# Kernel optimization log

Measured on AMD Instinct MI355X. Metric: run time of the kernel, lower is better.

The kernel has to match this reference:

```python
import jax, jax.numpy as jnp
import numpy as np

BS, SL, D_IN, D_MODEL, H = 4, 128, 512, 512, 8
DP = D_MODEL // H


def setup_inputs() -> dict:
    key = jax.random.key(0)
    ks = jax.random.split(key, 12)
    s = 0.02
    inp = {
        "q": jax.random.normal(ks[0], (BS, SL, D_IN), jnp.float32),
        "k": jax.random.normal(ks[1], (BS, SL, D_IN), jnp.float32),
        "v": jax.random.normal(ks[2], (BS, SL, D_IN), jnp.float32),
    }
    j = jnp.arange(SL)
    # mask[t, jk] = 1.0 for the zero-padded slots jk > t in the shuffled sequence for step t
    mask2d = (j[None, :] > j[:, None]).astype(jnp.float32)  # (SL, SL)
    inp["mask"] = mask2d[None, :, None, None, :]            # (1, SL, 1, 1, SL)
    for i, n in enumerate(["wq", "wk", "wv", "dense"]):
        din = D_IN if n != "dense" else D_MODEL
        inp[n + "_w"] = jax.random.normal(ks[3 + 2 * i], (din, D_MODEL), jnp.float32) * s
        inp[n + "_b"] = jnp.zeros((D_MODEL,), jnp.float32)
    return inp


def _shuffle_idx(key, sl):
    # Row t of returned idx: random permutation of [0..t-1], then t, then t+1.. (padding slots).
    u = jax.random.uniform(key, (sl, sl))
    j = jnp.arange(sl)
    t = j[:, None]
    sort_keys = jnp.where(j[None, :] < t, u, j[None, :].astype(jnp.float32) + 2.0)
    return jnp.argsort(sort_keys, axis=-1)  # (sl, sl) int32


def _split_heads_shuffled(x, idx, valid):
    # x: (bs, sl, d) -> (bs, sl, H, sl, DP); padding slots (j > t) zeroed like torch plc_holder
    bs, sl, d = x.shape
    xt = x[:, idx, :] * valid[None, :, :, None]  # (bs, sl, sl, d)
    xt = xt.reshape(bs, sl, sl, H, DP)
    return xt.transpose(0, 1, 3, 2, 4)


def reference(q, k, v, mask, wq_w, wq_b, wk_w, wk_b, wv_w, wv_b, dense_w, dense_b):
    bs, sl, _ = q.shape
    j = jnp.arange(sl)
    valid = (j[None, :] <= j[:, None]).astype(q.dtype)  # (sl, sl)
    pkey = jax.random.key(42)
    idx_q = _shuffle_idx(jax.random.fold_in(pkey, 0), sl)
    idx_k = _shuffle_idx(jax.random.fold_in(pkey, 1), sl)
    idx_v = _shuffle_idx(jax.random.fold_in(pkey, 2), sl)

    qp = q @ wq_w + wq_b
    kp = k @ wk_w + wk_b
    vp = v @ wv_w + wv_b

    qh = _split_heads_shuffled(qp, idx_q, valid)  # (bs, sl, H, sl, DP)
    kh = _split_heads_shuffled(kp, idx_k, valid)
    vh = _split_heads_shuffled(vp, idx_v, valid)

    logits = jnp.einsum('bthqd,bthkd->bthqk', qh, kh) / jnp.sqrt(jnp.float32(DP))
    logits = logits + mask * (-1e9)
    attn = jax.nn.softmax(logits, axis=-1)          # (bs, sl, H, sl, sl)
    ctx = jnp.einsum('bthqk,bthkd->bthqd', attn, vh)  # (bs, sl, H, sl, DP)

    ctx = ctx.transpose(0, 1, 3, 2, 4).reshape(bs, sl, sl, H * DP)
    eff = ctx[:, j, j, :]                           # query row t of step t (the token itself)
    out = eff @ dense_w + dense_b                   # (bs, sl, d_model); dropout p=0 -> identity
    return (out, attn)
```

## Files before the change

kernel.cpp:

```cpp
#include <hip/hip_runtime.h>
#include <stdint.h>


#define BSZ 4
#define SLEN 128
#define DMODEL 512
#define NHEAD 8
#define HDIM 64

typedef float f32x4_t __attribute__((ext_vector_type(4)));

__device__ __forceinline__ uint32_t rotl32(uint32_t v, int d) {
  return (v << d) | (v >> (32 - d));
}

__device__ __forceinline__ void tf2x32(uint32_t k0, uint32_t k1, uint32_t x0,
                                       uint32_t x1, uint32_t& y0, uint32_t& y1) {
  uint32_t ks2 = k0 ^ k1 ^ 0x1BD11BDAu;
  x0 += k0; x1 += k1;
#define TF_R(r) { x0 += x1; x1 = rotl32(x1, (r)); x1 ^= x0; }
  TF_R(13) TF_R(15) TF_R(26) TF_R(6)
  x0 += k1;  x1 += ks2 + 1u;
  TF_R(17) TF_R(29) TF_R(16) TF_R(24)
  x0 += ks2; x1 += k0 + 2u;
  TF_R(13) TF_R(15) TF_R(26) TF_R(6)
  x0 += k0;  x1 += k1 + 3u;
  TF_R(17) TF_R(29) TF_R(16) TF_R(24)
  x0 += k1;  x1 += ks2 + 4u;
  TF_R(13) TF_R(15) TF_R(26) TF_R(6)
  x0 += ks2; x1 += k0 + 5u;
#undef TF_R
  y0 = x0; y1 = x1;
}

__device__ __forceinline__ uint16_t f32_to_bf16(float v) {
  uint32_t x = __float_as_uint(v);
  return (uint16_t)((x + 0x7FFFu + ((x >> 16) & 1u)) >> 16);
}
__device__ __forceinline__ float bf16_to_f32(uint16_t b) {
  return __uint_as_float(((uint32_t)b) << 16);
}

__global__ __launch_bounds__(128) void idx_kernel(int* __restrict__ idx) {
  const int m = blockIdx.x;
  const int t = blockIdx.y;
  const int j = threadIdx.x;
  __shared__ float u[SLEN];
  uint32_t fk0, fk1;
  tf2x32(0u, 42u, 0u, (uint32_t)m, fk0, fk1);
  const int flat = t * SLEN + j;
  uint32_t y0, y1;
  tf2x32(fk0, fk1, 0u, (uint32_t)flat, y0, y1);
  uint32_t bits = y0 ^ y1;
  float uu = __uint_as_float((bits >> 9) | 0x3f800000u) - 1.0f;
  u[j] = uu;
  __syncthreads();
  int* row = idx + (m * SLEN + t) * SLEN;
  if (j >= t) {
    row[j] = j;
  } else {
    int rank = 0;
    for (int i = 0; i < t; ++i) {
      float ui = u[i];
      rank += ((ui < uu) || (ui == uu && i < j)) ? 1 : 0;
    }
    row[rank] = j;
  }
}

__device__ __forceinline__ void gemm512_body(const float* __restrict__ A,
                                             const float* __restrict__ W,
                                             const float* __restrict__ bias,
                                             float* __restrict__ C,
                                             float* As , float* Ws ) {
  const int tid = threadIdx.x;
  const int tx = tid & 15;
  const int ty = tid >> 4;
  const int row0 = blockIdx.y * 32, col0 = blockIdx.x * 64;
  const int lr = tid >> 2, lc = (tid & 3) << 2;
  const int wr = tid >> 4, wc = (tid & 15) << 2;
  float acc[2][4] = {};
  float4 av, wv;
  if (tid < 128) av = *(const float4*)(A + (size_t)(row0 + lr) * 512 + lc);
  wv = *(const float4*)(W + (size_t)wr * 512 + col0 + wc);
  for (int k0 = 0; k0 < 512; k0 += 16) {
    if (tid < 128) {
      As[lr * 17 + lc + 0] = av.x; As[lr * 17 + lc + 1] = av.y;
      As[lr * 17 + lc + 2] = av.z; As[lr * 17 + lc + 3] = av.w;
    }
    *(float4*)(Ws + wr * 64 + wc) = wv;
    __syncthreads();
    if (k0 + 16 < 512) {
      if (tid < 128) av = *(const float4*)(A + (size_t)(row0 + lr) * 512 + k0 + 16 + lc);
      wv = *(const float4*)(W + (size_t)(k0 + 16 + wr) * 512 + col0 + wc);
    }
#pragma unroll
    for (int kk = 0; kk < 16; ++kk) {
      float a0 = As[(ty * 2 + 0) * 17 + kk];
      float a1 = As[(ty * 2 + 1) * 17 + kk];
      float bvv[4];
#pragma unroll
      for (int jj = 0; jj < 4; ++jj) bvv[jj] = Ws[kk * 64 + tx * 4 + jj];
#pragma unroll
      for (int jj = 0; jj < 4; ++jj) {
        acc[0][jj] += a0 * bvv[jj];
        acc[1][jj] += a1 * bvv[jj];
      }
    }
    __syncthreads();
  }
#pragma unroll
  for (int i = 0; i < 2; ++i) {
    int r = row0 + ty * 2 + i, c = col0 + tx * 4;
    float4 o;
    o.x = acc[i][0] + bias[c + 0];
    o.y = acc[i][1] + bias[c + 1];
    o.z = acc[i][2] + bias[c + 2];
    o.w = acc[i][3] + bias[c + 3];
    *(float4*)(C + (size_t)r * 512 + c) = o;
  }
}

__global__ __launch_bounds__(256) void proj_kernel(
    const float* __restrict__ q, const float* __restrict__ k, const float* __restrict__ v,
    const float* __restrict__ wq, const float* __restrict__ wk, const float* __restrict__ wv,
    const float* __restrict__ bq, const float* __restrict__ bk, const float* __restrict__ bv,
    float* __restrict__ qp, float* __restrict__ kp, float* __restrict__ vp) {
  __shared__ float As[32 * 17];
  __shared__ float Ws[16 * 64];
  const float* A; const float* W; const float* B; float* C;
  if (blockIdx.z == 0)      { A = q; W = wq; B = bq; C = qp; }
  else if (blockIdx.z == 1) { A = k; W = wk; B = bk; C = kp; }
  else                      { A = v; W = wv; B = bv; C = vp; }
  gemm512_body(A, W, B, C, As, Ws);
}

__global__ __launch_bounds__(256) void dense_kernel(const float* __restrict__ A,
                                                    const float* __restrict__ W,
                                                    const float* __restrict__ B,
                                                    float* __restrict__ C) {
  __shared__ float As[32 * 17];
  __shared__ float Ws[16 * 64];
  gemm512_body(A, W, B, C, As, Ws);
}

__global__ __launch_bounds__(256) void sef_kernel(const float* __restrict__ qp,
                                                  const float* __restrict__ kp,
                                                  uint16_t* __restrict__ E,
                                                  float* __restrict__ Ft) {
  const int h = blockIdx.x, b = blockIdx.y, qc = blockIdx.z;
  const int tid = threadIdx.x;
  __shared__ float qs[32 * 36];
  __shared__ float ks[32 * 132];
  __shared__ float redm[32 * 16];
  __shared__ float csum[32 * 16];
  __shared__ float m32s[32];
  const float* qbase = qp + ((size_t)(b * SLEN + qc * 32)) * DMODEL + h * HDIM;
  const float* kbase = kp + ((size_t)b * SLEN) * DMODEL + h * HDIM;
  const int i0 = (tid >> 4) * 2, jg = tid & 15, j0 = jg * 8;
  float acc[2][8] = {};
  for (int d0 = 0; d0 < HDIM; d0 += 32) {
    __syncthreads();
    {
      int row = tid >> 3, c4 = (tid & 7) << 2;
      float4 a = *(const float4*)(qbase + (size_t)row * DMODEL + d0 + c4);
      qs[(c4 + 0) * 36 + row] = a.x; qs[(c4 + 1) * 36 + row] = a.y;
      qs[(c4 + 2) * 36 + row] = a.z; qs[(c4 + 3) * 36 + row] = a.w;
    }
    for (int it = 0; it < 4; ++it) {
      int flat = it * 256 + tid;
      int row = flat >> 3, c4 = (flat & 7) << 2;
      float4 bb = *(const float4*)(kbase + (size_t)row * DMODEL + d0 + c4);
      ks[(c4 + 0) * 132 + row] = bb.x; ks[(c4 + 1) * 132 + row] = bb.y;
      ks[(c4 + 2) * 132 + row] = bb.z; ks[(c4 + 3) * 132 + row] = bb.w;
    }
    __syncthreads();
    for (int d = 0; d < 32; ++d) {
      float a0 = qs[d * 36 + i0 + 0];
      float a1 = qs[d * 36 + i0 + 1];
      float4 ka = *(const float4*)(ks + d * 132 + j0);
      float4 kb = *(const float4*)(ks + d * 132 + j0 + 4);
      float bb[8] = {ka.x, ka.y, ka.z, ka.w, kb.x, kb.y, kb.z, kb.w};
#pragma unroll
      for (int c = 0; c < 8; ++c) {
        acc[0][c] += a0 * bb[c];
        acc[1][c] += a1 * bb[c];
      }
    }
  }
#pragma unroll
  for (int r = 0; r < 2; ++r) {
    float m = -3.402823466e38f;
#pragma unroll
    for (int c = 0; c < 8; ++c) {
      acc[r][c] *= 0.125f;
      m = fmaxf(m, acc[r][c]);
    }
    redm[(i0 + r) * 16 + jg] = m;
  }
  __syncthreads();
  if (tid < 32) {
    float m = redm[tid * 16];
#pragma unroll
    for (int g = 1; g < 16; ++g) m = fmaxf(m, redm[tid * 16 + g]);
    m32s[tid] = m;
  }
  __syncthreads();
  const int bh = b * NHEAD + h;
  uint16_t* Eb = E + (size_t)bh * SLEN * SLEN;
#pragma unroll
  for (int r = 0; r < 2; ++r) {
    const int grow = qc * 32 + i0 + r;
    const float m = m32s[i0 + r];
    float run = 0.f;
    ushort4 e0, e1;
    float ev;
    ev = __expf(acc[r][0] - m); e0.x = f32_to_bf16(ev); run += ev; acc[r][0] = run;
    ev = __expf(acc[r][1] - m); e0.y = f32_to_bf16(ev); run += ev; acc[r][1] = run;
    ev = __expf(acc[r][2] - m); e0.z = f32_to_bf16(ev); run += ev; acc[r][2] = run;
    ev = __expf(acc[r][3] - m); e0.w = f32_to_bf16(ev); run += ev; acc[r][3] = run;
    ev = __expf(acc[r][4] - m); e1.x = f32_to_bf16(ev); run += ev; acc[r][4] = run;
    ev = __expf(acc[r][5] - m); e1.y = f32_to_bf16(ev); run += ev; acc[r][5] = run;
    ev = __expf(acc[r][6] - m); e1.z = f32_to_bf16(ev); run += ev; acc[r][6] = run;
    ev = __expf(acc[r][7] - m); e1.w = f32_to_bf16(ev); run += ev; acc[r][7] = run;
    *(ushort4*)(Eb + (size_t)grow * SLEN + j0) = e0;
    *(ushort4*)(Eb + (size_t)grow * SLEN + j0 + 4) = e1;
    csum[(i0 + r) * 16 + jg] = run;
  }
  __syncthreads();
  float* Fb = Ft + (size_t)bh * SLEN * SLEN;
#pragma unroll
  for (int r = 0; r < 2; ++r) {
    const int grow = qc * 32 + i0 + r;
    float base = 0.f;
    for (int g = 0; g < 16; ++g) {
      if (g == jg) break;
      base += csum[(i0 + r) * 16 + g];
    }
#pragma unroll
    for (int c = 0; c < 8; ++c)
      Fb[(size_t)(j0 + c) * SLEN + grow] = 1.0f / (base + acc[r][c]);
  }
}

__global__ __launch_bounds__(256) void attn_kernel(const uint16_t* __restrict__ E,
                                                   const float* __restrict__ Ft,
                                                   const int* __restrict__ idx,
                                                   const float* __restrict__ vp,
                                                   float* __restrict__ attn_out,
                                                   float* __restrict__ eff) {
  const int h = blockIdx.x;
  const int tg = blockIdx.y;
  const int b = blockIdx.z;
  const int tid = threadIdx.x;
  const int wave = tid >> 6, lane = tid & 63;
  const int half = lane >> 5, l32 = lane & 31;
  const int bh = b * NHEAD + h;
  __shared__ __align__(16) uint16_t Es[SLEN * SLEN];
  __shared__ int iqs[8][SLEN];
  __shared__ int iks[8][SLEN];
  __shared__ int ivs[8][SLEN];
  __shared__ float Fsl[8][SLEN];
  {
    const uint4* src = (const uint4*)(E + (size_t)bh * SLEN * SLEN);
    uint4* dst = (uint4*)Es;
#pragma unroll
    for (int i = 0; i < 8; ++i) dst[i * 256 + tid] = src[i * 256 + tid];
  }
  {
    const int t0 = tg * 8;
#pragma unroll
    for (int ii = 0; ii < 4; ++ii) {
      int i = ii * 256 + tid;
      int s = i >> 7, j = i & 127;
      int t = t0 + s;
      iqs[s][j] = idx[(0 * SLEN + t) * SLEN + j];
      iks[s][j] = idx[(1 * SLEN + t) * SLEN + j];
      ivs[s][j] = idx[(2 * SLEN + t) * SLEN + j];
      Fsl[s][j] = Ft[((size_t)bh * SLEN + t) * SLEN + j];
    }
  }
  __syncthreads();
  const int k0 = l32 * 4;
  const int d = (wave << 4) + (lane >> 2);
  const int kg = lane & 3;
  const float* vb = vp + (size_t)b * SLEN * DMODEL + h * HDIM + d;
  for (int s = 0; s < 8; ++s) {
    const int t = tg * 8 + s;
    const int ikA = iks[s][k0], ikB = iks[s][k0 + 1], ikC = iks[s][k0 + 2], ikD = iks[s][k0 + 3];
    float4 cm;
    cm.x = (k0 + 0 <= t) ? 1.f : 0.f;
    cm.y = (k0 + 1 <= t) ? 1.f : 0.f;
    cm.z = (k0 + 2 <= t) ? 1.f : 0.f;
    cm.w = (k0 + 3 <= t) ? 1.f : 0.f;
    const float inv = 1.0f / (float)(t + 1);
    float* obase = attn_out + ((size_t)((b * SLEN + t) * NHEAD + h)) * SLEN * SLEN;
#pragma unroll 2
    for (int q8 = wave * 2; q8 < SLEN; q8 += 8) {
      const int qe = q8 + half;
      f32x4_t val;
      if (qe <= t) {
        const int iq = iqs[s][qe];
        const float f = Fsl[s][iq];
        const uint16_t* Er = Es + iq * SLEN;
        val.x = bf16_to_f32(Er[ikA]) * f * cm.x;
        val.y = bf16_to_f32(Er[ikB]) * f * cm.y;
        val.z = bf16_to_f32(Er[ikC]) * f * cm.z;
        val.w = bf16_to_f32(Er[ikD]) * f * cm.w;
      } else {
        val.x = inv * cm.x; val.y = inv * cm.y;
        val.z = inv * cm.z; val.w = inv * cm.w;
      }
      __builtin_nontemporal_store(val, (f32x4_t*)(obase + (size_t)qe * SLEN + k0));
    }
    {
      const uint16_t* Et = Es + t * SLEN;
      float acc = 0.f;
      int k = kg;
      for (; k + 28 <= t; k += 32) {
        float vv[8], ee[8];
#pragma unroll
        for (int i = 0; i < 8; ++i) {
          vv[i] = vb[(size_t)ivs[s][k + 4 * i] * DMODEL];
          ee[i] = bf16_to_f32(Et[iks[s][k + 4 * i]]);
        }
#pragma unroll
        for (int i = 0; i < 8; ++i) acc += ee[i] * vv[i];
      }
      for (; k <= t; k += 4)
        acc += bf16_to_f32(Et[iks[s][k]]) * vb[(size_t)ivs[s][k] * DMODEL];
      acc += __shfl_xor(acc, 1);
      acc += __shfl_xor(acc, 2);
      if (kg == 0)
        eff[((size_t)b * SLEN + t) * DMODEL + h * HDIM + d] = acc * Fsl[s][t];
    }
  }
}

extern "C" void kernel_launch(void* const* d_in, const int* in_sizes, int n_in,
                              void* d_out, int out_size, void* d_ws, size_t ws_size,
                              hipStream_t stream) {
  const float* q    = (const float*)d_in[0];
  const float* k    = (const float*)d_in[1];
  const float* v    = (const float*)d_in[2];
  const float* wq_w = (const float*)d_in[4];
  const float* wq_b = (const float*)d_in[5];
  const float* wk_w = (const float*)d_in[6];
  const float* wk_b = (const float*)d_in[7];
  const float* wv_w = (const float*)d_in[8];
  const float* wv_b = (const float*)d_in[9];
  const float* dw   = (const float*)d_in[10];
  const float* db   = (const float*)d_in[11];

  float* out  = (float*)d_out;
  float* attn = out + 262144;

  float* wsf = (float*)d_ws;
  uint16_t* E = (uint16_t*)wsf;
  int*   idx = (int*)(wsf + 262144);
  float* qp  = wsf + 311296;
  float* kp  = qp + 262144;
  float* vp  = kp + 262144;
  float* Ft  = vp + 262144;
  float* eff = Ft + 524288;
  (void)in_sizes; (void)n_in; (void)out_size; (void)ws_size;

  idx_kernel<<<dim3(3, 128, 1), 128, 0, stream>>>(idx);
  proj_kernel<<<dim3(8, 16, 3), 256, 0, stream>>>(q, k, v, wq_w, wk_w, wv_w,
                                                  wq_b, wk_b, wv_b, qp, kp, vp);
  sef_kernel<<<dim3(8, 4, 4), 256, 0, stream>>>(qp, kp, E, Ft);
  attn_kernel<<<dim3(8, 16, 4), 256, 0, stream>>>(E, Ft, idx, vp, attn, eff);
  dense_kernel<<<dim3(8, 16, 1), 256, 0, stream>>>(eff, dw, db, out);
}
```

Measured before the change: 362.4 us.

## Fuse dense projection into attention kernel via atomics and split per-timestep blocks

The attention kernel now runs one block per (head, timestep, batch) instead of one per group of 8 timesteps. It no longer stages the full 32KB E tile in LDS and reads E rows straight from global memory instead. The separate dense GEMM kernel is removed: each block multiplies its 64-wide context slice by the matching dense weight rows and atomically adds into an output buffer pre-filled with the bias. This raises parallelism and lowers LDS use, at the cost of uncached gathered global reads, redundant weight reads, an extra init launch, and float atomics with nondeterministic summation order.

New measurement: 368.2 us. About the same (+1.6%).

```diff
diff --git a/kernel.cpp b/kernel.cpp
--- a/kernel.cpp
+++ b/kernel.cpp
@@ -39,6 +39,12 @@
 }
 __device__ __forceinline__ float bf16_to_f32(uint16_t b) {
   return __uint_as_float(((uint32_t)b) << 16);
+}
+
+__global__ __launch_bounds__(512) void out_init_kernel(float* __restrict__ out,
+                                                       const float* __restrict__ db) {
+  const int i = blockIdx.x * 512 + threadIdx.x;
+  out[i] = db[i & (DMODEL - 1)];
 }
 
 __global__ __launch_bounds__(128) void idx_kernel(int* __restrict__ idx) {
@@ -132,15 +138,6 @@
   if (blockIdx.z == 0)      { A = q; W = wq; B = bq; C = qp; }
   else if (blockIdx.z == 1) { A = k; W = wk; B = bk; C = kp; }
   else                      { A = v; W = wv; B = bv; C = vp; }
-  gemm512_body(A, W, B, C, As, Ws);
-}
-
-__global__ __launch_bounds__(256) void dense_kernel(const float* __restrict__ A,
-                                                    const float* __restrict__ W,
-                                                    const float* __restrict__ B,
-                                                    float* __restrict__ C) {
-  __shared__ float As[32 * 17];
-  __shared__ float Ws[16 * 64];
   gemm512_body(A, W, B, C, As, Ws);
 }
 
@@ -247,93 +244,90 @@
                                                    const float* __restrict__ Ft,
                                                    const int* __restrict__ idx,
                                                    const float* __restrict__ vp,
+                                                   const float* __restrict__ dw,
                                                    float* __restrict__ attn_out,
-                                                   float* __restrict__ eff) {
-  const int h = blockIdx.x;
-  const int tg = blockIdx.y;
-  const int b = blockIdx.z;
+                                                   float* __restrict__ out) {
+  const int h = blockIdx.x, t = blockIdx.y, b = blockIdx.z;
   const int tid = threadIdx.x;
   const int wave = tid >> 6, lane = tid & 63;
   const int half = lane >> 5, l32 = lane & 31;
+  __shared__ int iqs[SLEN], iks[SLEN], ivs[SLEN];
+  __shared__ float Fs[SLEN];
+  __shared__ float effs[HDIM];
   const int bh = b * NHEAD + h;
-  __shared__ __align__(16) uint16_t Es[SLEN * SLEN];
-  __shared__ int iqs[8][SLEN];
-  __shared__ int iks[8][SLEN];
-  __shared__ int ivs[8][SLEN];
-  __shared__ float Fsl[8][SLEN];
+  if (tid < SLEN) {
+    iqs[tid] = idx[(0 * SLEN + t) * SLEN + tid];
+    iks[tid] = idx[(1 * SLEN + t) * SLEN + tid];
+    ivs[tid] = idx[(2 * SLEN + t) * SLEN + tid];
+    Fs[tid] = Ft[((size_t)bh * SLEN + t) * SLEN + tid];
+  }
+  __syncthreads();
+  const uint16_t* Eb = E + (size_t)bh * SLEN * SLEN;
+  const float inv = 1.0f / (float)(t + 1);
+  float* obase = attn_out + ((size_t)((b * SLEN + t) * NHEAD + h)) * SLEN * SLEN;
+  const int k0 = l32 * 4;
+  const int ikA = iks[k0], ikB = iks[k0 + 1], ikC = iks[k0 + 2], ikD = iks[k0 + 3];
+  float4 cm;
+  cm.x = (k0 + 0 <= t) ? 1.f : 0.f;
+  cm.y = (k0 + 1 <= t) ? 1.f : 0.f;
+  cm.z = (k0 + 2 <= t) ? 1.f : 0.f;
+  cm.w = (k0 + 3 <= t) ? 1.f : 0.f;
+#pragma unroll 2
+  for (int q8 = wave * 2; q8 < SLEN; q8 += 8) {
+    const int qe = q8 + half;
+    f32x4_t val;
+    if (qe <= t) {
+      const int iq = iqs[qe];
+      const float f = Fs[iq];
+      const uint16_t* Er = Eb + (size_t)iq * SLEN;
+      val.x = bf16_to_f32(Er[ikA]) * f * cm.x;
+      val.y = bf16_to_f32(Er[ikB]) * f * cm.y;
+      val.z = bf16_to_f32(Er[ikC]) * f * cm.z;
+      val.w = bf16_to_f32(Er[ikD]) * f * cm.w;
+    } else {
+      val.x = inv * cm.x; val.y = inv * cm.y;
+      val.z = inv * cm.z; val.w = inv * cm.w;
+    }
+    __builtin_nontemporal_store(val, (f32x4_t*)(obase + (size_t)qe * SLEN + k0));
+  }
   {
-    const uint4* src = (const uint4*)(E + (size_t)bh * SLEN * SLEN);
-    uint4* dst = (uint4*)Es;
-#pragma unroll
-    for (int i = 0; i < 8; ++i) dst[i * 256 + tid] = src[i * 256 + tid];
-  }
+    const int d = (wave << 4) + (lane >> 2);
+    const int kg = lane & 3;
+    const float* vb = vp + (size_t)b * SLEN * DMODEL + h * HDIM + d;
+    const uint16_t* Et = Eb + (size_t)t * SLEN;
+    float acc = 0.f;
+    int k = kg;
+    for (; k + 28 <= t; k += 32) {
+      float vv[8], ee[8];
+#pragma unroll
+      for (int i = 0; i < 8; ++i) {
+        vv[i] = vb[(size_t)ivs[k + 4 * i] * DMODEL];
+        ee[i] = bf16_to_f32(Et[iks[k + 4 * i]]);
+      }
+#pragma unroll
+      for (int i = 0; i < 8; ++i) acc += ee[i] * vv[i];
+    }
+    for (; k <= t; k += 4)
+      acc += bf16_to_f32(Et[iks[k]]) * vb[(size_t)ivs[k] * DMODEL];
+    acc += __shfl_xor(acc, 1);
+    acc += __shfl_xor(acc, 2);
+    if (kg == 0) effs[d] = acc * Fs[t];
+  }
+  __syncthreads();
   {
-    const int t0 = tg * 8;
-#pragma unroll
-    for (int ii = 0; ii < 4; ++ii) {
-      int i = ii * 256 + tid;
-      int s = i >> 7, j = i & 127;
-      int t = t0 + s;
-      iqs[s][j] = idx[(0 * SLEN + t) * SLEN + j];
-      iks[s][j] = idx[(1 * SLEN + t) * SLEN + j];
-      ivs[s][j] = idx[(2 * SLEN + t) * SLEN + j];
-      Fsl[s][j] = Ft[((size_t)bh * SLEN + t) * SLEN + j];
-    }
-  }
-  __syncthreads();
-  const int k0 = l32 * 4;
-  const int d = (wave << 4) + (lane >> 2);
-  const int kg = lane & 3;
-  const float* vb = vp + (size_t)b * SLEN * DMODEL + h * HDIM + d;
-  for (int s = 0; s < 8; ++s) {
-    const int t = tg * 8 + s;
-    const int ikA = iks[s][k0], ikB = iks[s][k0 + 1], ikC = iks[s][k0 + 2], ikD = iks[s][k0 + 3];
-    float4 cm;
-    cm.x = (k0 + 0 <= t) ? 1.f : 0.f;
-    cm.y = (k0 + 1 <= t) ? 1.f : 0.f;
-    cm.z = (k0 + 2 <= t) ? 1.f : 0.f;
-    cm.w = (k0 + 3 <= t) ? 1.f : 0.f;
-    const float inv = 1.0f / (float)(t + 1);
-    float* obase = attn_out + ((size_t)((b * SLEN + t) * NHEAD + h)) * SLEN * SLEN;
-#pragma unroll 2
-    for (int q8 = wave * 2; q8 < SLEN; q8 += 8) {
-      const int qe = q8 + half;
-      f32x4_t val;
-      if (qe <= t) {
-        const int iq = iqs[s][qe];
-        const float f = Fsl[s][iq];
-        const uint16_t* Er = Es + iq * SLEN;
-        val.x = bf16_to_f32(Er[ikA]) * f * cm.x;
-        val.y = bf16_to_f32(Er[ikB]) * f * cm.y;
-        val.z = bf16_to_f32(Er[ikC]) * f * cm.z;
-        val.w = bf16_to_f32(Er[ikD]) * f * cm.w;
-      } else {
-        val.x = inv * cm.x; val.y = inv * cm.y;
-        val.z = inv * cm.z; val.w = inv * cm.w;
-      }
-      __builtin_nontemporal_store(val, (f32x4_t*)(obase + (size_t)qe * SLEN + k0));
-    }
-    {
-      const uint16_t* Et = Es + t * SLEN;
-      float acc = 0.f;
-      int k = kg;
-      for (; k + 28 <= t; k += 32) {
-        float vv[8], ee[8];
-#pragma unroll
-        for (int i = 0; i < 8; ++i) {
-          vv[i] = vb[(size_t)ivs[s][k + 4 * i] * DMODEL];
-          ee[i] = bf16_to_f32(Et[iks[s][k + 4 * i]]);
-        }
-#pragma unroll
-        for (int i = 0; i < 8; ++i) acc += ee[i] * vv[i];
-      }
-      for (; k <= t; k += 4)
-        acc += bf16_to_f32(Et[iks[s][k]]) * vb[(size_t)ivs[s][k] * DMODEL];
-      acc += __shfl_xor(acc, 1);
-      acc += __shfl_xor(acc, 2);
-      if (kg == 0)
-        eff[((size_t)b * SLEN + t) * DMODEL + h * HDIM + d] = acc * Fsl[s][t];
-    }
+    const int c0 = tid * 2;
+    const float* wb = dw + (size_t)(h * HDIM) * DMODEL + c0;
+    float s0 = 0.f, s1 = 0.f;
+#pragma unroll 8
+    for (int d = 0; d < HDIM; ++d) {
+      const float e = effs[d];
+      const float2 wv = *(const float2*)(wb + (size_t)d * DMODEL);
+      s0 += e * wv.x;
+      s1 += e * wv.y;
+    }
+    float* orow = out + ((size_t)(b * SLEN + t)) * DMODEL;
+    atomicAdd(orow + c0 + 0, s0);
+    atomicAdd(orow + c0 + 1, s1);
   }
 }
 
@@ -362,13 +356,12 @@
   float* kp  = qp + 262144;
   float* vp  = kp + 262144;
   float* Ft  = vp + 262144;
-  float* eff = Ft + 524288;
   (void)in_sizes; (void)n_in; (void)out_size; (void)ws_size;
 
+  out_init_kernel<<<dim3(512, 1, 1), 512, 0, stream>>>(out, db);
   idx_kernel<<<dim3(3, 128, 1), 128, 0, stream>>>(idx);
   proj_kernel<<<dim3(8, 16, 3), 256, 0, stream>>>(q, k, v, wq_w, wk_w, wv_w,
                                                   wq_b, wk_b, wv_b, qp, kp, vp);
   sef_kernel<<<dim3(8, 4, 4), 256, 0, stream>>>(qp, kp, E, Ft);
-  attn_kernel<<<dim3(8, 16, 4), 256, 0, stream>>>(E, Ft, idx, vp, attn, eff);
-  dense_kernel<<<dim3(8, 16, 1), 256, 0, stream>>>(eff, dw, db, out);
-}
+  attn_kernel<<<dim3(8, 128, 4), 256, 0, stream>>>(E, Ft, idx, vp, dw, attn, out);
+}
```

## Fuse dense projection into attention kernel via per-head atomic accumulation

Applied to the files above, without the earlier changes.

Removes the separate dense GEMM kernel. Each attention block keeps its 8 context rows for one head in shared memory, multiplies them by that head's 64-row slice of the dense weight, and atomically adds the partial results into the output. A small init kernel first writes the bias into the output. This drops the eff round trip through global memory and one launch, at the cost of 8-way float atomics per output element and nondeterministic summation order.

Measured after the change: 352.0 us (median of 2 runs). 1.03x faster.

```diff
diff --git a/kernel.cpp b/kernel.cpp
--- a/kernel.cpp
+++ b/kernel.cpp
@@ -39,6 +39,12 @@
 }
 __device__ __forceinline__ float bf16_to_f32(uint16_t b) {
   return __uint_as_float(((uint32_t)b) << 16);
+}
+
+__global__ __launch_bounds__(512) void out_init_kernel(float* __restrict__ out,
+                                                       const float* __restrict__ db) {
+  const int i = blockIdx.x * 512 + threadIdx.x;
+  out[i] = db[i & (DMODEL - 1)];
 }
 
 __global__ __launch_bounds__(128) void idx_kernel(int* __restrict__ idx) {
@@ -132,15 +138,6 @@
   if (blockIdx.z == 0)      { A = q; W = wq; B = bq; C = qp; }
   else if (blockIdx.z == 1) { A = k; W = wk; B = bk; C = kp; }
   else                      { A = v; W = wv; B = bv; C = vp; }
-  gemm512_body(A, W, B, C, As, Ws);
-}
-
-__global__ __launch_bounds__(256) void dense_kernel(const float* __restrict__ A,
-                                                    const float* __restrict__ W,
-                                                    const float* __restrict__ B,
-                                                    float* __restrict__ C) {
-  __shared__ float As[32 * 17];
-  __shared__ float Ws[16 * 64];
   gemm512_body(A, W, B, C, As, Ws);
 }
 
@@ -247,8 +244,9 @@
                                                    const float* __restrict__ Ft,
                                                    const int* __restrict__ idx,
                                                    const float* __restrict__ vp,
+                                                   const float* __restrict__ dw,
                                                    float* __restrict__ attn_out,
-                                                   float* __restrict__ eff) {
+                                                   float* __restrict__ out) {
   const int h = blockIdx.x;
   const int tg = blockIdx.y;
   const int b = blockIdx.z;
@@ -261,6 +259,7 @@
   __shared__ int iks[8][SLEN];
   __shared__ int ivs[8][SLEN];
   __shared__ float Fsl[8][SLEN];
+  __shared__ float effs[8][HDIM];
   {
     const uint4* src = (const uint4*)(E + (size_t)bh * SLEN * SLEN);
     uint4* dst = (uint4*)Es;
@@ -331,8 +330,30 @@
         acc += bf16_to_f32(Et[iks[s][k]]) * vb[(size_t)ivs[s][k] * DMODEL];
       acc += __shfl_xor(acc, 1);
       acc += __shfl_xor(acc, 2);
-      if (kg == 0)
-        eff[((size_t)b * SLEN + t) * DMODEL + h * HDIM + d] = acc * Fsl[s][t];
+      if (kg == 0) effs[s][d] = acc * Fsl[s][t];
+    }
+  }
+  __syncthreads();
+  {
+    const int c0 = tid * 2;
+    const float* wb = dw + (size_t)(h * HDIM) * DMODEL + c0;
+    float s0[8] = {}, s1[8] = {};
+#pragma unroll 8
+    for (int dd = 0; dd < HDIM; ++dd) {
+      const float2 wv = *(const float2*)(wb + (size_t)dd * DMODEL);
+#pragma unroll
+      for (int s = 0; s < 8; ++s) {
+        const float e = effs[s][dd];
+        s0[s] += e * wv.x;
+        s1[s] += e * wv.y;
+      }
+    }
+    const int t0 = tg * 8;
+#pragma unroll
+    for (int s = 0; s < 8; ++s) {
+      float* orow = out + ((size_t)(b * SLEN + t0 + s)) * DMODEL;
+      atomicAdd(orow + c0 + 0, s0[s]);
+      atomicAdd(orow + c0 + 1, s1[s]);
     }
   }
 }
@@ -362,13 +383,12 @@
   float* kp  = qp + 262144;
   float* vp  = kp + 262144;
   float* Ft  = vp + 262144;
-  float* eff = Ft + 524288;
   (void)in_sizes; (void)n_in; (void)out_size; (void)ws_size;
 
+  out_init_kernel<<<dim3(512, 1, 1), 512, 0, stream>>>(out, db);
   idx_kernel<<<dim3(3, 128, 1), 128, 0, stream>>>(idx);
   proj_kernel<<<dim3(8, 16, 3), 256, 0, stream>>>(q, k, v, wq_w, wk_w, wv_w,
                                                   wq_b, wk_b, wv_b, qp, kp, vp);
   sef_kernel<<<dim3(8, 4, 4), 256, 0, stream>>>(qp, kp, E, Ft);
-  attn_kernel<<<dim3(8, 16, 4), 256, 0, stream>>>(E, Ft, idx, vp, attn, eff);
-  dense_kernel<<<dim3(8, 16, 1), 256, 0, stream>>>(eff, dw, db, out);
-}
+  attn_kernel<<<dim3(8, 16, 4), 256, 0, stream>>>(E, Ft, idx, vp, dw, attn, out);
+}
```
